# Performance work log

Measured on AMD Instinct MI355X. Metric: run time of the kernel, lower is better.

## Reference

```python
import jax, jax.numpy as jnp
import numpy as np

N_FOOD = 50000
N_NUT = 50000
E = 800000
D = 128      # embedding_dim == hidden_dim
H = 4        # heads
C = D // H   # per-head channels
L = 2        # num_layers
NEG_SLOPE = 0.2


def _gat_conv(x_src, x_dst, ei, Wsrc, Wdst, a_src, a_dst, bias, n_dst):
    """PyG GATConv (bipartite, no self loops, concat heads, no edge_dim)."""
    hs = (x_src @ Wsrc).reshape(-1, H, C)   # [Ns, H, C]
    hd = (x_dst @ Wdst).reshape(-1, H, C)   # [Nd, H, C]
    src, dst = ei[0], ei[1]
    alpha_s = jnp.einsum('nhc,hc->nh', hs, a_src)  # [Ns, H]
    alpha_d = jnp.einsum('nhc,hc->nh', hd, a_dst)  # [Nd, H]
    e = alpha_s[src] + alpha_d[dst]                # [E, H]
    e = jax.nn.leaky_relu(e, NEG_SLOPE)
    # segment softmax over edges grouped by destination node
    emax = jax.ops.segment_max(e, dst, num_segments=n_dst)
    emax = jnp.where(jnp.isfinite(emax), emax, 0.0)
    ex = jnp.exp(e - emax[dst])
    denom = jax.ops.segment_sum(ex, dst, num_segments=n_dst)
    alpha = ex / (denom[dst] + 1e-16)              # [E, H]
    msg = hs[src] * alpha[:, :, None]              # [E, H, C]
    out = jax.ops.segment_sum(msg, dst, num_segments=n_dst)
    return out.reshape(n_dst, H * C) + bias


def setup_inputs() -> dict:
    key = jax.random.key(0)
    ks = jax.random.split(key, 16)
    w = 1.0 / np.sqrt(D)
    a = 1.0 / np.sqrt(C)
    inp = {
        'x_food': jax.random.normal(ks[0], (N_FOOD, D), jnp.float32),
        'x_nut': jax.random.normal(ks[1], (N_NUT, D), jnp.float32),
        'Wsrc_fn': jax.random.normal(ks[2], (L, D, D), jnp.float32) * w,
        'Wdst_fn': jax.random.normal(ks[3], (L, D, D), jnp.float32) * w,
        'att_src_fn': jax.random.normal(ks[4], (L, H, C), jnp.float32) * a,
        'att_dst_fn': jax.random.normal(ks[5], (L, H, C), jnp.float32) * a,
        'bias_fn': jnp.zeros((L, D), jnp.float32),
        'Wsrc_nf': jax.random.normal(ks[6], (L, D, D), jnp.float32) * w,
        'Wdst_nf': jax.random.normal(ks[7], (L, D, D), jnp.float32) * w,
        'att_src_nf': jax.random.normal(ks[8], (L, H, C), jnp.float32) * a,
        'att_dst_nf': jax.random.normal(ks[9], (L, H, C), jnp.float32) * a,
        'bias_nf': jnp.zeros((L, D), jnp.float32),
        'ei_fn': jax.random.randint(ks[10], (2, E), 0, N_FOOD, jnp.int32),  # food -> nutrient
        'ei_nf': jax.random.randint(ks[11], (2, E), 0, N_NUT, jnp.int32),   # nutrient -> food
    }
    return inp


def reference(x_food, x_nut, Wsrc_fn, Wdst_fn, att_src_fn, att_dst_fn, bias_fn,
              Wsrc_nf, Wdst_nf, att_src_nf, att_dst_nf, bias_nf, ei_fn, ei_nf):
    h_food, h_nut = x_food, x_nut
    for l in range(L):
        # relation food --contains--> nutrient (dst = nutrient)
        out_nut = _gat_conv(h_food, h_nut, ei_fn, Wsrc_fn[l], Wdst_fn[l],
                            att_src_fn[l], att_dst_fn[l], bias_fn[l], N_NUT)
        # relation nutrient --contained_in--> food (dst = food)
        out_food = _gat_conv(h_nut, h_food, ei_nf, Wsrc_nf[l], Wdst_nf[l],
                             att_src_nf[l], att_dst_nf[l], bias_nf[l], N_FOOD)
        # dropout is identity at inference; ELU activation
        h_food = jax.nn.elu(out_food)
        h_nut = jax.nn.elu(out_nut)
    return jnp.stack([h_food, h_nut])  # [2, 50000, 128]
```

## Files before the change

### kernel.cpp

```cpp
#include <hip/hip_runtime.h>
#include <math.h>

#define NNODE 50000
#define NEDGE 800000
#define DIM   128
#define NHEAD 4
#define NTILE ((NNODE + 63) / 64)
#define NBUCK 196
#define ECHUNK 196
#define CAP   6144
#define LOG2E 1.44269504088896340736f
#define NODEBLK 12500

typedef __bf16 bf16x8 __attribute__((ext_vector_type(8)));
typedef float  f32x4  __attribute__((ext_vector_type(4)));
typedef float  f32x2  __attribute__((ext_vector_type(2)));
typedef _Float16 f16x8 __attribute__((ext_vector_type(8)));

static __device__ __forceinline__ void bfsplit(float x, ushort& hi, ushort& lo) {
    __bf16 h = (__bf16)x;
    float hf = (float)h;
    __bf16 l = (__bf16)(x - hf);
    hi = __builtin_bit_cast(unsigned short, h);
    lo = __builtin_bit_cast(unsigned short, l);
}
static __device__ __forceinline__ ushort f2h(float x) {
    _Float16 h = (_Float16)x;
    return __builtin_bit_cast(unsigned short, h);
}
static __device__ __forceinline__ unsigned encf(float f) {
    unsigned u = __builtin_bit_cast(unsigned, f);
    return (u >> 31) ? ~u : (u | 0x80000000u);
}
static __device__ __forceinline__ float decf(unsigned x) {
    unsigned u = (x >> 31) ? (x & 0x7fffffffu) : ~x;
    return __builtin_bit_cast(float, u);
}

__global__ __launch_bounds__(256) void bhist(const int* __restrict__ eA,
                                             const int* __restrict__ eB,
                                             int* __restrict__ bcnt) {
    int rel = (int)(blockIdx.x >= ECHUNK);
    const int* dstrow = (rel ? eB : eA) + NEDGE;
    int blk = blockIdx.x - rel * ECHUNK;
    __shared__ int hist[256];
    hist[threadIdx.x] = 0;
    __syncthreads();
    int base = blk * 4096;
    #pragma unroll
    for (int k = 0; k < 16; k++) {
        int e = base + k * 256 + threadIdx.x;
        if (e < NEDGE) atomicAdd(&hist[dstrow[e] >> 8], 1);
    }
    __syncthreads();
    int h = hist[threadIdx.x];
    if (h) atomicAdd(&bcnt[rel * 256 + threadIdx.x], h);
}

__global__ __launch_bounds__(256) void bscan(const int* __restrict__ bcnt,
                                             int* __restrict__ bko, int* __restrict__ bcur,
                                             int* __restrict__ ptrA, int* __restrict__ ptrB) {
    int rel = blockIdx.x;
    __shared__ int tmp[256];
    int t = threadIdx.x;
    int v = bcnt[rel * 256 + t];
    tmp[t] = v; __syncthreads();
    for (int off = 1; off < 256; off <<= 1) {
        int a = (t >= off) ? tmp[t - off] : 0; __syncthreads();
        tmp[t] += a; __syncthreads();
    }
    int excl = tmp[t] - v;
    bko[rel * 256 + t] = excl;
    bcur[rel * 256 + t] = excl;
    if (t == 255) (rel ? ptrB : ptrA)[NNODE] = tmp[255];
}

__global__ __launch_bounds__(256) void bscatter(const int* __restrict__ eA,
                                                const int* __restrict__ eB,
                                                int* __restrict__ bcur,
                                                unsigned* __restrict__ bktA,
                                                unsigned* __restrict__ bktB) {
    int rel = (int)(blockIdx.x >= ECHUNK);
    const int* ebase = rel ? eB : eA;
    unsigned* bkt = rel ? bktB : bktA;
    int blk = blockIdx.x - rel * ECHUNK;
    __shared__ int hist[256], bas[256], cur[256];
    hist[threadIdx.x] = 0;
    __syncthreads();
    int base = blk * 4096;
    #pragma unroll
    for (int k = 0; k < 16; k++) {
        int e = base + k * 256 + threadIdx.x;
        if (e < NEDGE) atomicAdd(&hist[ebase[NEDGE + e] >> 8], 1);
    }
    __syncthreads();
    int h = hist[threadIdx.x];
    bas[threadIdx.x] = h ? atomicAdd(&bcur[rel * 256 + threadIdx.x], h) : 0;
    cur[threadIdx.x] = 0;
    __syncthreads();
    #pragma unroll
    for (int k = 0; k < 16; k++) {
        int e = base + k * 256 + threadIdx.x;
        if (e < NEDGE) {
            int s = ebase[e], d = ebase[NEDGE + e];
            int b = d >> 8;
            int loc = atomicAdd(&cur[b], 1);
            bkt[bas[b] + loc] = ((unsigned)(d & 255) << 16) | (unsigned)s;
        }
    }
}

__global__ __launch_bounds__(256) void bsort(const unsigned* __restrict__ bktA,
                                             const unsigned* __restrict__ bktB,
                                             const int* __restrict__ bko,
                                             int* __restrict__ ptrA, int* __restrict__ ptrB,
                                             ushort* __restrict__ srcA, ushort* __restrict__ srcB) {
    int rel = (int)(blockIdx.x >= NBUCK);
    const unsigned* bkt = rel ? bktB : bktA;
    int* ptr   = rel ? ptrB : ptrA;
    ushort* srcs = rel ? srcB : srcA;
    int b = blockIdx.x - rel * NBUCK;
    int beg = bko[rel * 256 + b], end = bko[rel * 256 + b + 1];
    int cnt_e = end - beg;
    __shared__ int hist[256], excl[256], cur[256];
    __shared__ unsigned sorted[CAP];
    int t = threadIdx.x;
    hist[t] = 0;
    __syncthreads();
    for (int i = t; i < cnt_e; i += 256) atomicAdd(&hist[bkt[beg + i] >> 16], 1);
    __syncthreads();
    int v = hist[t];
    excl[t] = v; __syncthreads();
    for (int off = 1; off < 256; off <<= 1) {
        int a = (t >= off) ? excl[t - off] : 0; __syncthreads();
        excl[t] += a; __syncthreads();
    }
    int ex = excl[t] - v;
    int d = b * 256 + t;
    if (d < NNODE) ptr[d] = beg + ex;
    cur[t] = ex;
    __syncthreads();
    for (int i = t; i < cnt_e; i += 256) {
        unsigned u = bkt[beg + i];
        int dl = u >> 16;
        int p = atomicAdd(&cur[dl], 1);
        if (p < CAP) sorted[p] = u;
        else srcs[beg + p] = (ushort)(u & 0xffffu);
    }
    __syncthreads();
    int lim = cnt_e < CAP ? cnt_e : CAP;
    for (int i = t; i < lim; i += 256) {
        unsigned u = sorted[i];
        srcs[beg + i] = (ushort)(u & 0xffffu);
    }
}

__global__ void prep_wav(const float* __restrict__ Wsrc_fn, const float* __restrict__ a_src_fn,
                         const float* __restrict__ Wdst_fn, const float* __restrict__ a_dst_fn,
                         const float* __restrict__ Wsrc_nf, const float* __restrict__ a_src_nf,
                         const float* __restrict__ Wdst_nf, const float* __restrict__ a_dst_nf,
                         float* __restrict__ wav) {
    int call = blockIdx.x;
    int layer = call >> 1, which = call & 1;
    const float* Ws = which ? Wsrc_nf : Wsrc_fn;
    const float* as = which ? a_src_nf : a_src_fn;
    const float* Wd = which ? Wdst_fn : Wdst_nf;
    const float* ad = which ? a_dst_fn : a_dst_nf;
    Ws += layer * DIM * DIM; Wd += layer * DIM * DIM;
    as += layer * DIM; ad += layer * DIM;
    for (int it = threadIdx.x; it < 512; it += 256) {
        int k = it >> 2, h = it & 3;
        float s = 0.f, dv = 0.f;
        #pragma unroll 8
        for (int c = 0; c < 32; c++) {
            s  += Ws[k * DIM + h * 32 + c] * as[h * 32 + c];
            dv += Wd[k * DIM + h * 32 + c] * ad[h * 32 + c];
        }
        float* o = wav + (size_t)call * DIM * 8 + k * 8;
        o[h] = s; o[h + 4] = dv;
    }
}

__global__ __launch_bounds__(256, 4) void transform_kernel(
    const float* __restrict__ XA, const float* __restrict__ WA, const float* __restrict__ wavA,
    ushort* __restrict__ HSA, float* __restrict__ ASA, float* __restrict__ ADA,
    const float* __restrict__ XB, const float* __restrict__ WB, const float* __restrict__ wavB,
    ushort* __restrict__ HSB, float* __restrict__ ASB, float* __restrict__ ADB,
    unsigned* __restrict__ Mg, int nb)
{
    int rel = (int)(blockIdx.x >= (unsigned)nb);
    const float* X  = rel ? XB : XA;
    const float* W  = rel ? WB : WA;
    const float* wav = rel ? wavB : wavA;
    ushort* HS = rel ? HSB : HSA;
    float*  AS = rel ? ASB : ASA;
    float*  AD = rel ? ADB : ADA;

    __shared__ ushort WTh[64][136], WTl[64][136];
    __shared__ ushort hsb[32][72];
    __shared__ unsigned mloc[4];

    int vb = blockIdx.x - rel * nb;
    int half = vb & 1;
    int ch = half * 64;

    for (int i = threadIdx.x; i < 64 * DIM; i += 256) {
        int col = i & 63, k = i >> 6;
        ushort hi, lo; bfsplit(W[k * DIM + ch + col], hi, lo);
        WTh[col][k] = hi; WTl[col][k] = lo;
    }
    if (threadIdx.x < 4) mloc[threadIdx.x] = 0;

    const int wv = threadIdx.x >> 6, lane = threadIdx.x & 63;
    const int lm = lane & 15, lq = lane >> 4;
    const int r0 = wv * 16;
    const int tstride = nb >> 1;

    bf16x8 wvh[4], wvl[4];
    if (half == 0) {
        #pragma unroll
        for (int kc = 0; kc < 4; kc++) {
            int k0 = kc * 32 + lq * 8;
            #pragma unroll
            for (int j = 0; j < 8; j++) {
                float w = (lm < 8) ? wav[(k0 + j) * 8 + lm] : 0.f;
                __bf16 h = (__bf16)w;
                wvh[kc][j] = h;
                wvl[kc][j] = (__bf16)(w - (float)h);
            }
        }
    }
    __syncthreads();

    auto loadX = [&](int tile, float4* dst) {
        int myrow = tile * 64 + r0 + lm;
        int rowc = myrow < NNODE ? myrow : NNODE - 1;
        const float4* Xr = (const float4*)(X + (size_t)rowc * DIM);
        #pragma unroll
        for (int kc = 0; kc < 4; kc++) {
            dst[kc * 2]     = Xr[kc * 8 + lq * 2];
            dst[kc * 2 + 1] = Xr[kc * 8 + lq * 2 + 1];
        }
    };

    auto computeTile = [&](const float4* xv, int tile) {
        int row0 = tile * 64;
        f32x4 acc[4] = {{0,0,0,0},{0,0,0,0},{0,0,0,0},{0,0,0,0}};
        f32x4 accv = {0,0,0,0};
        #pragma unroll
        for (int kc = 0; kc < 4; kc++) {
            const float* fp = (const float*)&xv[kc * 2];
            bf16x8 ah, al;
            #pragma unroll
            for (int j = 0; j < 8; j++) {
                float x = fp[j];
                __bf16 h = (__bf16)x;
                ah[j] = h;
                al[j] = (__bf16)(x - (float)h);
            }
            int k0 = kc * 32 + lq * 8;
            #pragma unroll
            for (int ct = 0; ct < 4; ct++) {
                bf16x8 bh = *(const bf16x8*)&WTh[ct * 16 + lm][k0];
                bf16x8 bl = *(const bf16x8*)&WTl[ct * 16 + lm][k0];
                acc[ct] = __builtin_amdgcn_mfma_f32_16x16x32_bf16(al, bh, acc[ct], 0, 0, 0);
                acc[ct] = __builtin_amdgcn_mfma_f32_16x16x32_bf16(ah, bl, acc[ct], 0, 0, 0);
                acc[ct] = __builtin_amdgcn_mfma_f32_16x16x32_bf16(ah, bh, acc[ct], 0, 0, 0);
            }
            if (half == 0) {
                accv = __builtin_amdgcn_mfma_f32_16x16x32_bf16(al, wvh[kc], accv, 0, 0, 0);
                accv = __builtin_amdgcn_mfma_f32_16x16x32_bf16(ah, wvl[kc], accv, 0, 0, 0);
                accv = __builtin_amdgcn_mfma_f32_16x16x32_bf16(ah, wvh[kc], accv, 0, 0, 0);
            }
        }

        if (half == 0 && lm < 8) {
            accv *= LOG2E;
            float mx4 = -INFINITY;
            #pragma unroll
            for (int r = 0; r < 4; r++) {
                int row = row0 + r0 + lq * 4 + r;
                if (row < NNODE) {
                    if (lm < 4) AS[row * 4 + lm] = accv[r];
                    else        AD[row * 4 + (lm - 4)] = accv[r];
                }
                mx4 = fmaxf(mx4, accv[r]);
            }
            if (lm < 4) atomicMax(&mloc[lm], encf(mx4));
        }

        #pragma unroll
        for (int p = 0; p < 2; p++) {
            __syncthreads();
            if ((wv >> 1) == p) {
                #pragma unroll
                for (int ct = 0; ct < 4; ct++) {
                    #pragma unroll
                    for (int r = 0; r < 4; r++)
                        hsb[(r0 & 31) + lq * 4 + r][ct * 16 + lm] = f2h(acc[ct][r]);
                }
            }
            __syncthreads();
            int lr = (int)threadIdx.x >> 3, off = ((int)threadIdx.x & 7) * 8;
            int rg = row0 + p * 32 + lr;
            if (rg < NNODE)
                *(uint4*)(HS + (size_t)rg * DIM + ch + off) = *(const uint4*)&hsb[lr][off];
        }
    };

    float4 xa[8], xb[8];
    int tile = vb >> 1;
    loadX(tile, xa);
    while (tile < NTILE) {
        if (tile + tstride < NTILE) loadX(tile + tstride, xb);
        computeTile(xa, tile);
        tile += tstride;
        if (tile >= NTILE) break;
        if (tile + tstride < NTILE) loadX(tile + tstride, xa);
        computeTile(xb, tile);
        tile += tstride;
    }

    __syncthreads();
    if (half == 0 && threadIdx.x < 4)
        atomicMax(&Mg[rel * 4 + threadIdx.x], mloc[threadIdx.x]);
}

__global__ __launch_bounds__(256) void agg_kernel(
    const ushort* __restrict__ HSA, const float* __restrict__ ASA, const float* __restrict__ ADA,
    const int* __restrict__ ptrA, const ushort* __restrict__ srcA,
    const float* __restrict__ biasA, float* __restrict__ outA,
    const ushort* __restrict__ HSB, const float* __restrict__ ASB, const float* __restrict__ ADB,
    const int* __restrict__ ptrB, const ushort* __restrict__ srcB,
    const float* __restrict__ biasB, float* __restrict__ outB,
    const unsigned* __restrict__ Mg)
{
    unsigned idx = blockIdx.x;
    int g   = (idx >> 2) & 1;
    int sub = (int)((idx >> 3) << 2) | (int)(idx & 3);
    int rel = (int)(sub >= NODEBLK);
    int bid = sub - rel * NODEBLK;

    const uint4* HS4 = (const uint4*)(rel ? HSB : HSA);
    const float* AS = rel ? ASB : ASA;
    const float* AD = rel ? ADB : ADA;
    const ushort* srcs = rel ? srcB : srcA;
    const int* ptr = rel ? ptrB : ptrA;
    const float* bias = rel ? biasB : biasA;
    float* out = rel ? outB : outA;

    int wave = threadIdx.x >> 6, lane = threadIdx.x & 63;
    int d = bid * 4 + wave;

    int q  = lane >> 3;
    int li = lane & 7;
    int hh = g * 2 + (li >> 2);

    float ad_h = AD[d * 4 + hh];
    float mm = decf(Mg[rel * 4 + hh]) + ad_h;
    mm = fmaxf(mm, 0.2f * mm);

    int e0 = ptr[d], e1 = ptr[d + 1];

    float acc[8] = {0.f,0.f,0.f,0.f,0.f,0.f,0.f,0.f};
    float l = 0.f;
    int rowoff = g * 8 + li;

    int e = e0;
    for (; e + 16 <= e1; e += 16) {
        int sA = srcs[e + q], sB = srcs[e + 8 + q];
        uint4 uA = HS4[sA * 16 + rowoff];
        uint4 uB = HS4[sB * 16 + rowoff];
        float aA = AS[sA * 4 + hh], aB = AS[sB * 4 + hh];
        float vA = aA + ad_h; vA = fmaxf(vA, 0.2f * vA);
        float vB = aB + ad_h; vB = fmaxf(vB, 0.2f * vB);
        float pA = __builtin_amdgcn_exp2f(vA - mm);
        float pB = __builtin_amdgcn_exp2f(vB - mm);
        l += pA + pB;
        f16x8 hA = __builtin_bit_cast(f16x8, uA);
        f16x8 hB = __builtin_bit_cast(f16x8, uB);
        #pragma unroll
        for (int j = 0; j < 8; j++) {
            acc[j] = __builtin_fmaf((float)hA[j], pA, acc[j]);
            acc[j] = __builtin_fmaf((float)hB[j], pB, acc[j]);
        }
    }
    for (; e + 8 <= e1; e += 8) {
        int s = srcs[e + q];
        uint4 u = HS4[s * 16 + rowoff];
        float a = AS[s * 4 + hh];
        float v = a + ad_h; v = fmaxf(v, 0.2f * v);
        float p = __builtin_amdgcn_exp2f(v - mm);
        l += p;
        f16x8 h = __builtin_bit_cast(f16x8, u);
        #pragma unroll
        for (int j = 0; j < 8; j++)
            acc[j] = __builtin_fmaf((float)h[j], p, acc[j]);
    }
    if (e < e1) {
        int ee = e + q;
        bool act = ee < e1;
        int eidx = act ? ee : e1 - 1;
        int s = srcs[eidx];
        uint4 u = HS4[s * 16 + rowoff];
        float a = AS[s * 4 + hh];
        float v = a + ad_h; v = fmaxf(v, 0.2f * v);
        float p = __builtin_amdgcn_exp2f(v - mm);
        p = act ? p : 0.f;
        l += p;
        f16x8 h = __builtin_bit_cast(f16x8, u);
        #pragma unroll
        for (int j = 0; j < 8; j++)
            acc[j] = __builtin_fmaf((float)h[j], p, acc[j]);
    }

    #pragma unroll
    for (int j = 0; j < 8; j++) {
        acc[j] += __shfl_xor(acc[j], 8, 64);
        acc[j] += __shfl_xor(acc[j], 16, 64);
        acc[j] += __shfl_xor(acc[j], 32, 64);
    }
    l += __shfl_xor(l, 8, 64);
    l += __shfl_xor(l, 16, 64);
    l += __shfl_xor(l, 32, 64);

    if (q == 0) {
        float inv = 1.f / (l + 1e-16f);
        const float4* b4 = (const float4*)(bias + g * 64) + li * 2;
        float4 b0 = b4[0], b1 = b4[1];
        float o[8];
        o[0] = acc[0] * inv + b0.x; o[1] = acc[1] * inv + b0.y;
        o[2] = acc[2] * inv + b0.z; o[3] = acc[3] * inv + b0.w;
        o[4] = acc[4] * inv + b1.x; o[5] = acc[5] * inv + b1.y;
        o[6] = acc[6] * inv + b1.z; o[7] = acc[7] * inv + b1.w;
        #pragma unroll
        for (int j = 0; j < 8; j++)
            o[j] = o[j] > 0.f ? o[j] : __expf(o[j]) - 1.f;
        float4* o4 = (float4*)(out + (size_t)d * DIM + g * 64) + li * 2;
        o4[0] = make_float4(o[0], o[1], o[2], o[3]);
        o4[1] = make_float4(o[4], o[5], o[6], o[7]);
    }
}

extern "C" void kernel_launch(void* const* d_in, const int* in_sizes, int n_in,
                              void* d_out, int out_size, void* d_ws, size_t ws_size,
                              hipStream_t stream) {
    const float* x_food      = (const float*)d_in[0];
    const float* x_nut       = (const float*)d_in[1];
    const float* Wsrc_fn     = (const float*)d_in[2];
    const float* Wdst_fn     = (const float*)d_in[3];
    const float* att_src_fn  = (const float*)d_in[4];
    const float* att_dst_fn  = (const float*)d_in[5];
    const float* bias_fn     = (const float*)d_in[6];
    const float* Wsrc_nf     = (const float*)d_in[7];
    const float* Wdst_nf     = (const float*)d_in[8];
    const float* att_src_nf  = (const float*)d_in[9];
    const float* att_dst_nf  = (const float*)d_in[10];
    const float* bias_nf     = (const float*)d_in[11];
    const int*   ei_fn       = (const int*)d_in[12];
    const int*   ei_nf       = (const int*)d_in[13];
    float* out = (float*)d_out;

    char* ws = (char*)d_ws;
    size_t off = 0;
    auto alloc_f = [&](size_t n) { float* p = (float*)(ws + off); off += n * 4; return p; };
    auto alloc_i = [&](size_t n) { int* p = (int*)(ws + off); off += n * 4; return p; };
    auto alloc_u = [&](size_t n) { ushort* p = (ushort*)(ws + off); off += n * 2; return p; };

    float* B_food = alloc_f((size_t)NNODE * DIM);
    float* B_nut  = alloc_f((size_t)NNODE * DIM);
    ushort* HS_fn = alloc_u((size_t)NNODE * DIM);
    ushort* HS_nf = alloc_u((size_t)NNODE * DIM);
    float* AS_fn  = alloc_f(NNODE * NHEAD);
    float* AS_nf  = alloc_f(NNODE * NHEAD);
    float* AD_fn  = alloc_f(NNODE * NHEAD);
    float* AD_nf  = alloc_f(NNODE * NHEAD);
    float* wav    = alloc_f(4 * DIM * 8);
    int* ptr_fn   = alloc_i(50004);
    int* ptr_nf   = alloc_i(50004);
    ushort* srcs_fn = alloc_u(NEDGE);
    ushort* srcs_nf = alloc_u(NEDGE);
    int* bcnt     = alloc_i(512);
    unsigned* Mbuf = (unsigned*)alloc_i(16);
    int* bko      = alloc_i(512);
    int* bcur     = alloc_i(512);
    unsigned* bkt_fn = (unsigned*)B_food;
    unsigned* bkt_nf = (unsigned*)B_nut;

    hipMemsetAsync(bcnt, 0, (512 + 16) * 4, stream);
    bhist<<<2 * ECHUNK, 256, 0, stream>>>(ei_fn, ei_nf, bcnt);
    bscan<<<2, 256, 0, stream>>>(bcnt, bko, bcur, ptr_fn, ptr_nf);
    bscatter<<<2 * ECHUNK, 256, 0, stream>>>(ei_fn, ei_nf, bcur, bkt_fn, bkt_nf);
    bsort<<<2 * NBUCK, 256, 0, stream>>>(bkt_fn, bkt_nf, bko, ptr_fn, ptr_nf,
                                         srcs_fn, srcs_nf);

    prep_wav<<<4, 256, 0, stream>>>(Wsrc_fn, att_src_fn, Wdst_fn, att_dst_fn,
                                    Wsrc_nf, att_src_nf, Wdst_nf, att_dst_nf, wav);

    const int WL = DIM * DIM;
    const int TNB = 512;
    const int AGRID = 2 * 2 * NODEBLK;
    float* wav0 = wav;
    float* wav1 = wav + DIM * 8;
    float* wav2 = wav + 2 * DIM * 8;
    float* wav3 = wav + 3 * DIM * 8;

    transform_kernel<<<2 * TNB, 256, 0, stream>>>(
        x_food, Wsrc_fn, wav0, HS_fn, AS_fn, AD_nf,
        x_nut,  Wsrc_nf, wav1, HS_nf, AS_nf, AD_fn, Mbuf, TNB);
    agg_kernel<<<AGRID, 256, 0, stream>>>(
        HS_fn, AS_fn, AD_fn, ptr_fn, srcs_fn, bias_fn, B_nut,
        HS_nf, AS_nf, AD_nf, ptr_nf, srcs_nf, bias_nf, B_food, Mbuf);

    transform_kernel<<<2 * TNB, 256, 0, stream>>>(
        B_food, Wsrc_fn + WL, wav2, HS_fn, AS_fn, AD_nf,
        B_nut,  Wsrc_nf + WL, wav3, HS_nf, AS_nf, AD_fn, Mbuf + 8, TNB);
    agg_kernel<<<AGRID, 256, 0, stream>>>(
        HS_fn, AS_fn, AD_fn, ptr_fn, srcs_fn, bias_fn + DIM, out + (size_t)NNODE * DIM,
        HS_nf, AS_nf, AD_nf, ptr_nf, srcs_nf, bias_nf + DIM, out, Mbuf + 8);
}
```

Measured before the change: 440.9 us.

## Map two destination nodes per wave in aggregation, halving grid size

The aggregation kernel now splits each 64-lane wave into two 32-lane halves, each handling its own destination node with 4 edge slots of 8 lanes. The block count halves accordingly, and the main loop processes 16 edges in four loads per lane to keep enough gathers in flight. The final reduction drops one shuffle stage. This lowers per-node launch and reduction overhead, but each node now gets fewer lanes for its edges, and the two halves of a wave can diverge when their degrees differ.

```diff
diff --git a/kernel.cpp b/kernel.cpp
--- a/kernel.cpp
+++ b/kernel.cpp
@@ -10,7 +10,7 @@
 #define ECHUNK 196
 #define CAP   6144
 #define LOG2E 1.44269504088896340736f
-#define NODEBLK 12500
+#define NODEOCT (NNODE / 8)
 
 typedef __bf16 bf16x8 __attribute__((ext_vector_type(8)));
 typedef float  f32x4  __attribute__((ext_vector_type(4)));
@@ -338,8 +338,8 @@
     unsigned idx = blockIdx.x;
     int g   = (idx >> 2) & 1;
     int sub = (int)((idx >> 3) << 2) | (int)(idx & 3);
-    int rel = (int)(sub >= NODEBLK);
-    int bid = sub - rel * NODEBLK;
+    int rel = (int)(sub >= NODEOCT);
+    int bid = sub - rel * NODEOCT;
 
     const uint4* HS4 = (const uint4*)(rel ? HSB : HSA);
     const float* AS = rel ? ASB : ASA;
@@ -350,11 +350,12 @@
     float* out = rel ? outB : outA;
 
     int wave = threadIdx.x >> 6, lane = threadIdx.x & 63;
-    int d = bid * 4 + wave;
-
-    int q  = lane >> 3;
+    int h32 = lane >> 5;
+    int q  = (lane >> 3) & 3;
     int li = lane & 7;
     int hh = g * 2 + (li >> 2);
+    int d = bid * 8 + wave * 2 + h32;
+    int rowoff = g * 8 + li;
 
     float ad_h = AD[d * 4 + hh];
     float mm = decf(Mg[rel * 4 + hh]) + ad_h;
@@ -364,11 +365,40 @@
 
     float acc[8] = {0.f,0.f,0.f,0.f,0.f,0.f,0.f,0.f};
     float l = 0.f;
-    int rowoff = g * 8 + li;
 
     int e = e0;
     for (; e + 16 <= e1; e += 16) {
-        int sA = srcs[e + q], sB = srcs[e + 8 + q];
+        int s0 = srcs[e + q],     s1 = srcs[e + 4 + q];
+        int s2 = srcs[e + 8 + q], s3 = srcs[e + 12 + q];
+        uint4 u0 = HS4[s0 * 16 + rowoff];
+        uint4 u1 = HS4[s1 * 16 + rowoff];
+        uint4 u2 = HS4[s2 * 16 + rowoff];
+        uint4 u3 = HS4[s3 * 16 + rowoff];
+        float a0 = AS[s0 * 4 + hh], a1 = AS[s1 * 4 + hh];
+        float a2 = AS[s2 * 4 + hh], a3 = AS[s3 * 4 + hh];
+        float v0 = a0 + ad_h; v0 = fmaxf(v0, 0.2f * v0);
+        float v1 = a1 + ad_h; v1 = fmaxf(v1, 0.2f * v1);
+        float v2 = a2 + ad_h; v2 = fmaxf(v2, 0.2f * v2);
+        float v3 = a3 + ad_h; v3 = fmaxf(v3, 0.2f * v3);
+        float p0 = __builtin_amdgcn_exp2f(v0 - mm);
+        float p1 = __builtin_amdgcn_exp2f(v1 - mm);
+        float p2 = __builtin_amdgcn_exp2f(v2 - mm);
+        float p3 = __builtin_amdgcn_exp2f(v3 - mm);
+        l += (p0 + p1) + (p2 + p3);
+        f16x8 h0 = __builtin_bit_cast(f16x8, u0);
+        f16x8 h1 = __builtin_bit_cast(f16x8, u1);
+        f16x8 h2 = __builtin_bit_cast(f16x8, u2);
+        f16x8 h3 = __builtin_bit_cast(f16x8, u3);
+        #pragma unroll
+        for (int j = 0; j < 8; j++) {
+            acc[j] = __builtin_fmaf((float)h0[j], p0, acc[j]);
+            acc[j] = __builtin_fmaf((float)h1[j], p1, acc[j]);
+            acc[j] = __builtin_fmaf((float)h2[j], p2, acc[j]);
+            acc[j] = __builtin_fmaf((float)h3[j], p3, acc[j]);
+        }
+    }
+    for (; e + 8 <= e1; e += 8) {
+        int sA = srcs[e + q], sB = srcs[e + 4 + q];
         uint4 uA = HS4[sA * 16 + rowoff];
         uint4 uB = HS4[sB * 16 + rowoff];
         float aA = AS[sA * 4 + hh], aB = AS[sB * 4 + hh];
@@ -385,19 +415,7 @@
             acc[j] = __builtin_fmaf((float)hB[j], pB, acc[j]);
         }
     }
-    for (; e + 8 <= e1; e += 8) {
-        int s = srcs[e + q];
-        uint4 u = HS4[s * 16 + rowoff];
-        float a = AS[s * 4 + hh];
-        float v = a + ad_h; v = fmaxf(v, 0.2f * v);
-        float p = __builtin_amdgcn_exp2f(v - mm);
-        l += p;
-        f16x8 h = __builtin_bit_cast(f16x8, u);
-        #pragma unroll
-        for (int j = 0; j < 8; j++)
-            acc[j] = __builtin_fmaf((float)h[j], p, acc[j]);
-    }
-    if (e < e1) {
+    for (; e < e1; e += 4) {
         int ee = e + q;
         bool act = ee < e1;
         int eidx = act ? ee : e1 - 1;
@@ -418,11 +436,9 @@
     for (int j = 0; j < 8; j++) {
         acc[j] += __shfl_xor(acc[j], 8, 64);
         acc[j] += __shfl_xor(acc[j], 16, 64);
-        acc[j] += __shfl_xor(acc[j], 32, 64);
     }
     l += __shfl_xor(l, 8, 64);
     l += __shfl_xor(l, 16, 64);
-    l += __shfl_xor(l, 32, 64);
 
     if (q == 0) {
         float inv = 1.f / (l + 1e-16f);
@@ -499,7 +515,7 @@
 
     const int WL = DIM * DIM;
     const int TNB = 512;
-    const int AGRID = 2 * 2 * NODEBLK;
+    const int AGRID = 2 * 2 * NODEOCT;
     float* wav0 = wav;
     float* wav1 = wav + DIM * 8;
     float* wav2 = wav + 2 * DIM * 8;
```

Result: faster. 396.1 us (-10.2%).
